# Optimization experiments

Measured on AMD Instinct MI355X. Metric: run time of the kernel, lower is better.

Reference implementation:

```python
import jax, jax.numpy as jnp
from jax import lax
import numpy as np

B, S, V, E, H, K = 128, 512, 32000, 128, 128, 32  # H = hidden_dim//2 per direction
START, END = 30, 31


def _lstm_dir(x, h0, c0, W_ih, W_hh, b):
    # x: [S, B, E]; PyTorch gate order: i, f, g, o
    def step(carry, xt):
        h, c = carry
        gates = xt @ W_ih.T + h @ W_hh.T + b  # [B, 4H]
        i, f, g, o = jnp.split(gates, 4, axis=1)
        c = jax.nn.sigmoid(f) * c + jax.nn.sigmoid(i) * jnp.tanh(g)
        h = jax.nn.sigmoid(o) * jnp.tanh(c)
        return (h, c), h
    _, hs = lax.scan(step, (h0, c0), x)
    return hs  # [S, B, H]


def _get_features(sentence, embed_table, W_ih_f, W_hh_f, b_ih_f, b_hh_f,
                  W_ih_b, W_hh_b, b_ih_b, b_hh_b, W_out, b_out, h0, c0):
    emb = embed_table[sentence]            # [B, S, E]
    x = emb.transpose(1, 0, 2)             # [S, B, E]
    hf = _lstm_dir(x, h0[0], c0[0], W_ih_f, W_hh_f, b_ih_f + b_hh_f)
    hb = _lstm_dir(x[::-1], h0[1], c0[1], W_ih_b, W_hh_b, b_ih_b + b_hh_b)[::-1]
    out = jnp.concatenate([hf, hb], axis=-1).transpose(1, 0, 2)  # [B, S, 2H]
    return out @ W_out.T + b_out           # [B, S, K]


def _numerator(feats, tags, transitions):
    b = tags.shape[0]
    start = jnp.full((b, 1), START, dtype=tags.dtype)
    ext = jnp.concatenate([start, tags], axis=1)  # [B, S+1]
    trans = transitions[ext[:, :-1], ext[:, 1:]].sum(axis=1)
    emit = jnp.take_along_axis(feats, tags[:, :, None], axis=2)[..., 0].sum(axis=1)
    return trans + emit + transitions[tags[:, -1], END]


def _denominator(feats, transitions):
    b, _, k = feats.shape
    init = jnp.full((b, k), -10000.0, feats.dtype).at[:, START].set(0.0)
    def step(alpha, feat):
        # alpha[b, prev]; transitions[next, prev] (as in the torch code)
        new = jax.nn.logsumexp(alpha[:, None, :] + transitions[None, :, :], axis=2) + feat
        return new, None
    alpha, _ = lax.scan(step, init, feats.transpose(1, 0, 2))
    return jax.nn.logsumexp(alpha + transitions[:, END][None, :], axis=1)


def setup_inputs():
    key = jax.random.key(0)
    ks = jax.random.split(key, 16)
    n = lambda k, shape, s=0.1: jax.random.normal(k, shape, jnp.float32) * s
    sentence = jax.random.randint(ks[0], (B, S), 0, V)
    tags = jax.random.randint(ks[1], (B, S), 0, START)
    transitions = n(ks[13], (K, K), 0.1)
    transitions = transitions.at[:, START].set(-10000.0).at[END, :].set(-10000.0)
    return dict(
        sentence=sentence, tags=tags,
        embed_table=n(ks[2], (V, E), 1.0),
        W_ih_f=n(ks[3], (4 * H, E)), W_hh_f=n(ks[4], (4 * H, H)),
        b_ih_f=n(ks[5], (4 * H,)), b_hh_f=n(ks[6], (4 * H,)),
        W_ih_b=n(ks[7], (4 * H, E)), W_hh_b=n(ks[8], (4 * H, H)),
        b_ih_b=n(ks[9], (4 * H,)), b_hh_b=n(ks[10], (4 * H,)),
        W_out=n(ks[11], (K, 2 * H)), b_out=n(ks[12], (K,)),
        transitions=transitions,
        h0=n(ks[14], (2, B, H)), c0=n(ks[15], (2, B, H)),
    )


def reference(sentence, tags, embed_table, W_ih_f, W_hh_f, b_ih_f, b_hh_f,
              W_ih_b, W_hh_b, b_ih_b, b_hh_b, W_out, b_out, transitions, h0, c0):
    feats = _get_features(sentence, embed_table, W_ih_f, W_hh_f, b_ih_f, b_hh_f,
                          W_ih_b, W_hh_b, b_ih_b, b_hh_b, W_out, b_out, h0, c0)
    num = _numerator(feats, tags, transitions)
    den = _denominator(feats, transitions)
    return jnp.mean(num - den)
```

## Files before the change

kernel.cpp:

```cpp
#include <hip/hip_runtime.h>

typedef unsigned int uint;
typedef __fp16 half2_t __attribute__((ext_vector_type(2)));
typedef __fp16 half8_t __attribute__((ext_vector_type(8)));
typedef float floatx4 __attribute__((ext_vector_type(4)));

#define SEQ 512
#define BATCH 128
#define HID 128
#define NTAG 32
#define START_TAG 30
#define END_TAG 31

__device__ __forceinline__ float fdot2(uint a, uint b, float c) {
  return __builtin_amdgcn_fdot2(__builtin_bit_cast(half2_t, a),
                                __builtin_bit_cast(half2_t, b), c, false);
}
__device__ __forceinline__ uint packh2(float a, float b) {
  half2_t h = __builtin_amdgcn_cvt_pkrtz(a, b);
  return __builtin_bit_cast(uint, h);
}
__device__ __forceinline__ float frcp(float x) { return __builtin_amdgcn_rcpf(x); }
__device__ __forceinline__ float fsig(float x) { return frcp(1.f + __expf(-x)); }
__device__ __forceinline__ float ftanh(float x) { return 1.f - 2.f * frcp(1.f + __expf(2.f * x)); }
__device__ __forceinline__ float fexp2(float x) { return __builtin_amdgcn_exp2f(x); }
__device__ __forceinline__ float flog2(float x) { return __builtin_amdgcn_logf(x); }

__global__ __launch_bounds__(256) void prep_kernel(
    const float* __restrict__ Wihf, const float* __restrict__ Whhf,
    const float* __restrict__ bihf, const float* __restrict__ bhhf,
    const float* __restrict__ Wihb, const float* __restrict__ Whhb,
    const float* __restrict__ bihb, const float* __restrict__ bhhb,
    const float* __restrict__ Wout,
    uint* __restrict__ wihI, uint* __restrict__ whh,
    uint* __restrict__ woutp, float* __restrict__ biasI)
{
  int idx = blockIdx.x * 256 + threadIdx.x;
  if (idx < 65536) {
    int d = idx >> 15, rem = idx & 32767;
    int n = rem >> 6, dw = rem & 63;
    int m = n >> 2, q = n & 3;
    int g = q * 128 + m;
    const float* W = d ? Wihb : Wihf;
    wihI[idx] = packh2(W[g * 128 + 2 * dw], W[g * 128 + 2 * dw + 1]);
  }
  int i2 = idx - 65536;
  if (i2 >= 0 && i2 < 65536) {
    int d = i2 >> 15, rem = i2 & 32767;
    int g = rem >> 6, dw = rem & 63;
    const float* W = d ? Whhb : Whhf;
    whh[i2] = packh2(W[g * 128 + 2 * dw], W[g * 128 + 2 * dw + 1]);
  }
  int i3 = idx - 131072;
  if (i3 >= 0 && i3 < 4096) {
    int k = i3 >> 7, dw = i3 & 127;
    float a, b2;
    if (dw < 64) { a = Wout[k * 256 + 2 * dw]; b2 = Wout[k * 256 + 2 * dw + 1]; }
    else { int j = dw - 64; a = Wout[k * 256 + 128 + 2 * j]; b2 = Wout[k * 256 + 128 + 2 * j + 1]; }
    woutp[i3] = packh2(a, b2);
  }
  int i4 = idx - 135168;
  if (i4 >= 0 && i4 < 1024) {
    int d = i4 >> 9, n = i4 & 511;
    int g = (n & 3) * 128 + (n >> 2);
    biasI[i4] = d ? (bihb[g] + bhhb[g]) : (bihf[g] + bhhf[g]);
  }
}

__global__ __launch_bounds__(256, 2) void gemmx_kernel(
    const int* __restrict__ sentence, const float* __restrict__ embed,
    const uint* __restrict__ wihI, const float* __restrict__ biasI,
    uint* __restrict__ gatex, int chunk)
{
  int blk = blockIdx.x;
  int tl = blk & 127, nb = (blk >> 7) & 3, d = blk >> 9;
  int t = chunk * 128 + tl;
  int s = d ? (511 - t) : t;
  __shared__ int tok[128];
  int tid = threadIdx.x;
  if (tid < 128) tok[tid] = sentence[tid * SEQ + s];
  __syncthreads();

  int w = tid >> 6, lane = tid & 63;
  int q = lane >> 4, r = lane & 15;
  int wr = w >> 1, wc = w & 1;
  int r0 = wr * 64;
  int c0 = nb * 128 + wc * 64;

  floatx4 acc[4][4];
#pragma unroll
  for (int i = 0; i < 4; ++i)
#pragma unroll
    for (int j = 0; j < 4; ++j) acc[i][j] = (floatx4){0.f, 0.f, 0.f, 0.f};

  const float4* aptr[4];
#pragma unroll
  for (int i = 0; i < 4; ++i)
    aptr[i] = (const float4*)(embed + (size_t)tok[r0 + i * 16 + r] * HID) + q * 2;
  const uint4* bptr[4];
#pragma unroll
  for (int j = 0; j < 4; ++j)
    bptr[j] = (const uint4*)(wihI + ((size_t)d * 512 + c0 + j * 16 + r) * 64) + q;

#pragma unroll
  for (int kc = 0; kc < 4; ++kc) {
    half8_t af[4], bf[4];
#pragma unroll
    for (int i = 0; i < 4; ++i) {
      float4 x0 = aptr[i][kc * 8];
      float4 x1 = aptr[i][kc * 8 + 1];
      uint4 u;
      u.x = packh2(x0.x, x0.y); u.y = packh2(x0.z, x0.w);
      u.z = packh2(x1.x, x1.y); u.w = packh2(x1.z, x1.w);
      af[i] = __builtin_bit_cast(half8_t, u);
    }
#pragma unroll
    for (int j = 0; j < 4; ++j)
      bf[j] = __builtin_bit_cast(half8_t, bptr[j][kc * 4]);
#pragma unroll
    for (int i = 0; i < 4; ++i)
#pragma unroll
      for (int j = 0; j < 4; ++j)
        acc[i][j] = __builtin_amdgcn_mfma_f32_16x16x32_f16(af[i], bf[j], acc[i][j], 0, 0, 0);
  }

  __fp16* gat = ((__fp16*)gatex) + (size_t)d * 16384 * 512;
#pragma unroll
  for (int j = 0; j < 4; ++j) {
    int n = c0 + j * 16 + r;
    float bb = biasI[d * 512 + n];
#pragma unroll
    for (int i = 0; i < 4; ++i) {
      int rb = r0 + i * 16 + q * 4;
#pragma unroll
      for (int reg = 0; reg < 4; ++reg) {
        float v = acc[i][j][reg] + bb;
        gat[((size_t)(tl * 128 + rb + reg)) * 512 + n] = (__fp16)v;
      }
    }
  }
}

__global__ __launch_bounds__(256, 1) void lstm_kernel(
    const uint* __restrict__ gatex, const uint* __restrict__ whh,
    const float* __restrict__ h0, const float* __restrict__ c0,
    float* __restrict__ statec, uint* __restrict__ hh, int chunk)
{
  const int wg = blockIdx.x;
  const int d = wg >> 7, b = wg & 127;
  const int tid = threadIdx.x;
  const int w = tid >> 6, lane = tid & 63;
  const int hp = lane >> 5, r = lane & 31;
  const int m = w * 32 + r;

  __shared__ __align__(16) __fp16 hist[128][128];
  __shared__ uint occupancy_pad[16384];
  if (chunk == -12345) occupancy_pad[tid] = (uint)tid;

  const uint4* wh4 = (const uint4*)(whh + (size_t)d * 512 * 64);
  uint4 wreg[4][8];
#pragma unroll
  for (int q = 0; q < 4; ++q) {
    const uint4* row = wh4 + (q * 128 + m) * 16 + hp * 8;
#pragma unroll
    for (int i = 0; i < 8; ++i) wreg[q][i] = row[i];
  }

  float c = (chunk == 0) ? c0[(size_t)(d * 128 + b) * 128 + m]
                         : statec[(size_t)(d * 128 + b) * 128 + m];

  if (tid < 64) {
    uint* h127 = (uint*)&hist[127][0];
    if (chunk == 0) {
      float2 hv = ((const float2*)(h0 + (size_t)(d * 128 + b) * 128))[tid];
      h127[tid] = packh2(hv.x, hv.y);
    } else {
      int sprev = d ? (511 - (chunk * 128 - 1)) : (chunk * 128 - 1);
      h127[tid] = hh[((size_t)(d * 512 + sprev) * 128 + b) * 64 + tid];
    }
  }
  const uint* gx0 = gatex + (size_t)d * 4194304 + (size_t)b * 256 + 2 * m;
  uint2 gx = *(const uint2*)(gx0);
  __syncthreads();

  for (int tl = 0; tl < 128; ++tl) {
    uint2 gxn = gx;
    if (tl < 127) gxn = *(const uint2*)(gx0 + (size_t)(tl + 1) * 32768);

    float a0 = 0.f, a1 = 0.f, a2 = 0.f, a3 = 0.f;
    const uint4* z4 = (const uint4*)(&hist[(tl + 127) & 127][hp * 64]);
#pragma unroll
    for (int i = 0; i < 8; ++i) {
      uint4 z = z4[i];
      a0 = fdot2(z.x, wreg[0][i].x, a0);
      a0 = fdot2(z.y, wreg[0][i].y, a0);
      a0 = fdot2(z.z, wreg[0][i].z, a0);
      a0 = fdot2(z.w, wreg[0][i].w, a0);
      a1 = fdot2(z.x, wreg[1][i].x, a1);
      a1 = fdot2(z.y, wreg[1][i].y, a1);
      a1 = fdot2(z.z, wreg[1][i].z, a1);
      a1 = fdot2(z.w, wreg[1][i].w, a1);
      a2 = fdot2(z.x, wreg[2][i].x, a2);
      a2 = fdot2(z.y, wreg[2][i].y, a2);
      a2 = fdot2(z.z, wreg[2][i].z, a2);
      a2 = fdot2(z.w, wreg[2][i].w, a2);
      a3 = fdot2(z.x, wreg[3][i].x, a3);
      a3 = fdot2(z.y, wreg[3][i].y, a3);
      a3 = fdot2(z.z, wreg[3][i].z, a3);
      a3 = fdot2(z.w, wreg[3][i].w, a3);
    }
    a0 += __shfl_xor(a0, 32);
    a1 += __shfl_xor(a1, 32);
    a2 += __shfl_xor(a2, 32);
    a3 += __shfl_xor(a3, 32);

    half2_t g01 = __builtin_bit_cast(half2_t, gx.x);
    half2_t g23 = __builtin_bit_cast(half2_t, gx.y);
    a0 += (float)g01[0];
    a1 += (float)g01[1];
    a2 += (float)g23[0];
    a3 += (float)g23[1];

    float ig = fsig(a0);
    float fg = fsig(a1);
    float gg = ftanh(a2);
    float og = fsig(a3);
    c = fg * c + ig * gg;
    float hv = og * ftanh(c);

    if (hp == 0) hist[tl][m] = (__fp16)hv;
    gx = gxn;
    __syncthreads();
  }

  statec[(size_t)(d * 128 + b) * 128 + m] = c;

  int base = chunk * 128;
  for (int i = tid; i < 2048; i += 256) {
    int sl = i >> 4, q4 = i & 15;
    int s = d ? (511 - (base + sl)) : (base + sl);
    *(uint4*)(&hh[((size_t)(d * 512 + s) * 128 + b) * 64 + q4 * 4]) =
        *(const uint4*)((const uint*)&hist[sl][0] + q4 * 4);
  }
}

__global__ __launch_bounds__(256) void outproj_kernel(
    const uint* __restrict__ hh, const uint* __restrict__ woutp,
    const float* __restrict__ bout, float* __restrict__ feats)
{
  __shared__ __align__(16) uint4 zrow[8][32];
  __shared__ __align__(16) uint4 wlds[32][32];
  int tid = threadIdx.x;
  for (int j = tid; j < 1024; j += 256) {
    int k = j >> 5, i = j & 31;
    wlds[i][k] = ((const uint4*)woutp)[j];
  }
  int rl = tid >> 5, q = tid & 31;
  int row = blockIdx.x * 8 + rl;
  int b = row >> 9, s = row & 511;
  const uint4* hf4 = (const uint4*)(hh + ((size_t)s * BATCH + b) * 64);
  const uint4* hb4 = (const uint4*)(hh + ((size_t)(SEQ + s) * BATCH + b) * 64);
  zrow[rl][q] = (q < 16) ? hf4[q] : hb4[q - 16];
  __syncthreads();
  int k = q;
  float acc = bout[k];
#pragma unroll
  for (int i = 0; i < 32; ++i) {
    uint4 z = zrow[rl][i];
    uint4 wv = wlds[i][k];
    acc = fdot2(z.x, wv.x, acc);
    acc = fdot2(z.y, wv.y, acc);
    acc = fdot2(z.z, wv.z, acc);
    acc = fdot2(z.w, wv.w, acc);
  }
  feats[(size_t)row * 32 + k] = acc;
}

__global__ __launch_bounds__(64) void crf_num_kernel(
    const int* __restrict__ tags, const float* __restrict__ feats,
    const float* __restrict__ trans, float* __restrict__ num)
{
  int b = blockIdx.x, l = threadIdx.x;
  const int* tb = tags + b * SEQ;
  float acc = 0.f;
  for (int s = l; s < SEQ; s += 64) {
    int tg = tb[s];
    int pv = (s == 0) ? START_TAG : tb[s - 1];
    acc += trans[pv * NTAG + tg] + feats[((size_t)b * SEQ + s) * NTAG + tg];
  }
#pragma unroll
  for (int msk = 1; msk < 64; msk <<= 1) acc += __shfl_xor(acc, msk);
  if (l == 0) num[b] = acc + trans[tb[SEQ - 1] * NTAG + END_TAG];
}

__global__ __launch_bounds__(64) void crf_seg_kernel(
    const float* __restrict__ feats, const float* __restrict__ trans,
    uint* __restrict__ segP, float* __restrict__ segL)
{
  const float L2E = 1.4426950408889634f;
  int blk = blockIdx.x;
  int b = blk >> 5, j = blk & 31;
  int tstart = 1 + 16 * j;
  int nsteps = (j == 31) ? 15 : 16;
  int lane = threadIdx.x;
  int c = lane & 15, q = lane >> 4;

  half8_t afr[2];
#pragma unroll
  for (int rt = 0; rt < 2; ++rt) {
    const float* trow = trans + (rt * 16 + c) * 32 + q * 8;
    float e[8];
#pragma unroll
    for (int i = 0; i < 8; ++i) e[i] = fexp2(trow[i] * L2E);
    uint4 u;
    u.x = packh2(e[0], e[1]); u.y = packh2(e[2], e[3]);
    u.z = packh2(e[4], e[5]); u.w = packh2(e[6], e[7]);
    afr[rt] = __builtin_bit_cast(half8_t, u);
  }
  half8_t bfr[2];
#pragma unroll
  for (int ct = 0; ct < 2; ++ct) {
    uint4 u;
    uint vals[8];
#pragma unroll
    for (int i = 0; i < 8; ++i)
      vals[i] = ((q * 8 + i) == (ct * 16 + c)) ? 0x3C00u : 0u;
    u.x = vals[0] | (vals[1] << 16);
    u.y = vals[2] | (vals[3] << 16);
    u.z = vals[4] | (vals[5] << 16);
    u.w = vals[6] | (vals[7] << 16);
    bfr[ct] = __builtin_bit_cast(half8_t, u);
  }

  __shared__ __fp16 P16[32 * 36];

  const float* fb = feats + ((size_t)b * SEQ + tstart) * NTAG;
  float Lacc = 0.f;
  float4 pre0 = *(const float4*)(fb + q * 4);
  float4 pre1 = *(const float4*)(fb + 16 + q * 4);

  for (int s = 0; s < nsteps; ++s) {
    float4 f0 = pre0, f1 = pre1;
    if (s + 1 < nsteps) {
      pre0 = *(const float4*)(fb + (s + 1) * 32 + q * 4);
      pre1 = *(const float4*)(fb + (s + 1) * 32 + 16 + q * 4);
    }
    floatx4 z4 = (floatx4){0.f, 0.f, 0.f, 0.f};
    floatx4 c00 = __builtin_amdgcn_mfma_f32_16x16x32_f16(afr[0], bfr[0], z4, 0, 0, 0);
    floatx4 c01 = __builtin_amdgcn_mfma_f32_16x16x32_f16(afr[0], bfr[1], z4, 0, 0, 0);
    floatx4 c10 = __builtin_amdgcn_mfma_f32_16x16x32_f16(afr[1], bfr[0], z4, 0, 0, 0);
    floatx4 c11 = __builtin_amdgcn_mfma_f32_16x16x32_f16(afr[1], bfr[1], z4, 0, 0, 0);
    float pf0[4], pf1[4];
    pf0[0] = fexp2(f0.x * L2E); pf0[1] = fexp2(f0.y * L2E);
    pf0[2] = fexp2(f0.z * L2E); pf0[3] = fexp2(f0.w * L2E);
    pf1[0] = fexp2(f1.x * L2E); pf1[1] = fexp2(f1.y * L2E);
    pf1[2] = fexp2(f1.z * L2E); pf1[3] = fexp2(f1.w * L2E);
    float v00[4], v01[4], v10[4], v11[4];
#pragma unroll
    for (int rg = 0; rg < 4; ++rg) {
      v00[rg] = c00[rg] * pf0[rg];
      v01[rg] = c01[rg] * pf0[rg];
      v10[rg] = c10[rg] * pf1[rg];
      v11[rg] = c11[rg] * pf1[rg];
    }
    float mx = 0.f;
#pragma unroll
    for (int rg = 0; rg < 4; ++rg)
      mx = fmaxf(mx, fmaxf(fmaxf(v00[rg], v01[rg]), fmaxf(v10[rg], v11[rg])));
    uint ub = (uint)__builtin_amdgcn_readfirstlane((int)__builtin_bit_cast(uint, mx));
    int e = (int)((ub >> 23) & 255u);
    Lacc += (float)(e - 127);
    float sc = __builtin_bit_cast(float, (uint)((254 - e) << 23));

    __syncthreads();
    {
      uint2 wv2;
      wv2.x = packh2(v00[0] * sc, v00[1] * sc);
      wv2.y = packh2(v00[2] * sc, v00[3] * sc);
      *(uint2*)(&P16[c * 36 + q * 4]) = wv2;
      wv2.x = packh2(v10[0] * sc, v10[1] * sc);
      wv2.y = packh2(v10[2] * sc, v10[3] * sc);
      *(uint2*)(&P16[c * 36 + 16 + q * 4]) = wv2;
      wv2.x = packh2(v01[0] * sc, v01[1] * sc);
      wv2.y = packh2(v01[2] * sc, v01[3] * sc);
      *(uint2*)(&P16[(16 + c) * 36 + q * 4]) = wv2;
      wv2.x = packh2(v11[0] * sc, v11[1] * sc);
      wv2.y = packh2(v11[2] * sc, v11[3] * sc);
      *(uint2*)(&P16[(16 + c) * 36 + 16 + q * 4]) = wv2;
    }
    __syncthreads();
    {
      uint2 lo0 = *(const uint2*)(&P16[c * 36 + q * 8]);
      uint2 hi0 = *(const uint2*)(&P16[c * 36 + q * 8 + 4]);
      uint4 u0; u0.x = lo0.x; u0.y = lo0.y; u0.z = hi0.x; u0.w = hi0.y;
      bfr[0] = __builtin_bit_cast(half8_t, u0);
      uint2 lo1 = *(const uint2*)(&P16[(16 + c) * 36 + q * 8]);
      uint2 hi1 = *(const uint2*)(&P16[(16 + c) * 36 + q * 8 + 4]);
      uint4 u1; u1.x = lo1.x; u1.y = lo1.y; u1.z = hi1.x; u1.w = hi1.y;
      bfr[1] = __builtin_bit_cast(half8_t, u1);
    }
  }
  __syncthreads();
  uint* gp = segP + (size_t)blk * 512;
  if (lane < 32) {
    int i = lane;
#pragma unroll
    for (int tp = 0; tp < 16; ++tp) {
      uint lo = (uint)__builtin_bit_cast(unsigned short, P16[(2 * tp) * 36 + i]);
      uint hi = (uint)__builtin_bit_cast(unsigned short, P16[(2 * tp + 1) * 36 + i]);
      gp[i * 16 + tp] = lo | (hi << 16);
    }
  }
  if (lane == 0) segL[blk] = Lacc;
}

__global__ __launch_bounds__(64) void crf_comb_kernel(
    const float* __restrict__ feats, const float* __restrict__ trans,
    const uint* __restrict__ segP, const float* __restrict__ segL,
    float* __restrict__ den)
{
  const float L2E = 1.4426950408889634f, LN2 = 0.6931471805599453f;
  int b = blockIdx.x, l = threadIdx.x;
  int i = l & 31, hp = l >> 5;
  const float* fb = feats + (size_t)b * SEQ * NTAG;

  float sT = 0.f;
  for (int p = 0; p < 32; ++p) sT += fexp2(trans[i * 32 + p] * L2E);
  float v = (1.f + sT) * fexp2(fb[i] * L2E);
  float L = -10000.f * L2E;

  float vo = __shfl_xor(v, 1);
  uint pv = (i & 1) ? packh2(vo, v) : packh2(v, vo);

  const uint* gp0 = segP + (size_t)b * 32 * 512 + i * 16 + hp * 8;
  uint4 ra = *(const uint4*)(gp0);
  uint4 rb = *(const uint4*)(gp0 + 4);

  for (int seg = 0; seg < 32; ++seg) {
    uint4 ca = ra, cb = rb;
    if (seg + 1 < 32) {
      ra = *(const uint4*)(gp0 + (seg + 1) * 512);
      rb = *(const uint4*)(gp0 + (seg + 1) * 512 + 4);
    }
    float g0 = __shfl(__builtin_bit_cast(float, pv), hp * 16 + 0);
    float g1 = __shfl(__builtin_bit_cast(float, pv), hp * 16 + 2);
    float g2 = __shfl(__builtin_bit_cast(float, pv), hp * 16 + 4);
    float g3 = __shfl(__builtin_bit_cast(float, pv), hp * 16 + 6);
    float g4 = __shfl(__builtin_bit_cast(float, pv), hp * 16 + 8);
    float g5 = __shfl(__builtin_bit_cast(float, pv), hp * 16 + 10);
    float g6 = __shfl(__builtin_bit_cast(float, pv), hp * 16 + 12);
    float g7 = __shfl(__builtin_bit_cast(float, pv), hp * 16 + 14);
    float acc = 0.f;
    acc = fdot2(__builtin_bit_cast(uint, g0), ca.x, acc);
    acc = fdot2(__builtin_bit_cast(uint, g1), ca.y, acc);
    acc = fdot2(__builtin_bit_cast(uint, g2), ca.z, acc);
    acc = fdot2(__builtin_bit_cast(uint, g3), ca.w, acc);
    acc = fdot2(__builtin_bit_cast(uint, g4), cb.x, acc);
    acc = fdot2(__builtin_bit_cast(uint, g5), cb.y, acc);
    acc = fdot2(__builtin_bit_cast(uint, g6), cb.z, acc);
    acc = fdot2(__builtin_bit_cast(uint, g7), cb.w, acc);
    float sm = acc + __shfl_xor(acc, 32);
    uint ub = (uint)__builtin_amdgcn_readfirstlane((int)__builtin_bit_cast(uint, sm));
    int e = (int)((ub >> 23) & 255u);
    L += (float)(e - 127) + segL[b * 32 + seg];
    float sc = __builtin_bit_cast(float, (uint)((254 - e) << 23));
    v = sm * sc;
    float vo2 = __shfl_xor(v, 1);
    pv = (i & 1) ? packh2(vo2, v) : packh2(v, vo2);
  }
  float wv = v * fexp2(trans[i * 32 + END_TAG] * L2E);
#pragma unroll
  for (int msk = 1; msk <= 16; msk <<= 1) wv += __shfl_xor(wv, msk);
  if (l == 0) den[b] = (L + flog2(wv)) * LN2;
}

__global__ __launch_bounds__(128) void final_kernel(
    const float* __restrict__ num, const float* __restrict__ den,
    float* __restrict__ out)
{
  int tid = threadIdx.x;
  float v = num[tid] - den[tid];
#pragma unroll
  for (int msk = 1; msk < 64; msk <<= 1) v += __shfl_xor(v, msk);
  __shared__ float tmp[2];
  if ((tid & 63) == 0) tmp[tid >> 6] = v;
  __syncthreads();
  if (tid == 0) out[0] = (tmp[0] + tmp[1]) * (1.f / 128.f);
}

extern "C" void kernel_launch(void* const* d_in, const int* in_sizes, int n_in,
                              void* d_out, int out_size, void* d_ws, size_t ws_size,
                              hipStream_t stream)
{
  const int* sentence = (const int*)d_in[0];
  const int* tags = (const int*)d_in[1];
  const float* embed = (const float*)d_in[2];
  const float* Wihf = (const float*)d_in[3];
  const float* Whhf = (const float*)d_in[4];
  const float* bihf = (const float*)d_in[5];
  const float* bhhf = (const float*)d_in[6];
  const float* Wihb = (const float*)d_in[7];
  const float* Whhb = (const float*)d_in[8];
  const float* bihb = (const float*)d_in[9];
  const float* bhhb = (const float*)d_in[10];
  const float* Wout = (const float*)d_in[11];
  const float* bout = (const float*)d_in[12];
  const float* trans = (const float*)d_in[13];
  const float* h0 = (const float*)d_in[14];
  const float* c0 = (const float*)d_in[15];
  float* out = (float*)d_out;

  char* ws = (char*)d_ws;
  uint* wihI = (uint*)(ws + 0);
  uint* whh = (uint*)(ws + 262144);
  uint* woutp = (uint*)(ws + 524288);
  float* biasI = (float*)(ws + 540672);
  float* numb = (float*)(ws + 544768);
  float* denb = (float*)(ws + 545280);
  float* statec = (float*)(ws + 545792);
  uint* hh = (uint*)(ws + 1048576);
  uint* gatex = (uint*)(ws + 34603008);
  float* feats = (float*)(ws + 34603008);
  uint* segP = (uint*)(ws + 42991616);
  float* segL = (float*)(ws + 51380224);

  hipLaunchKernelGGL(prep_kernel, dim3(532), dim3(256), 0, stream,
                     Wihf, Whhf, bihf, bhhf, Wihb, Whhb, bihb, bhhb, Wout,
                     wihI, whh, woutp, biasI);
  for (int c = 0; c < 4; ++c) {
    hipLaunchKernelGGL(gemmx_kernel, dim3(1024), dim3(256), 0, stream,
                       sentence, embed, wihI, biasI, gatex, c);
    hipLaunchKernelGGL(lstm_kernel, dim3(256), dim3(256), 0, stream,
                       gatex, whh, h0, c0, statec, hh, c);
  }
  hipLaunchKernelGGL(outproj_kernel, dim3(8192), dim3(256), 0, stream,
                     hh, woutp, bout, feats);
  hipLaunchKernelGGL(crf_num_kernel, dim3(128), dim3(64), 0, stream,
                     tags, feats, trans, numb);
  hipLaunchKernelGGL(crf_seg_kernel, dim3(4096), dim3(64), 0, stream,
                     feats, trans, segP, segL);
  hipLaunchKernelGGL(crf_comb_kernel, dim3(128), dim3(64), 0, stream,
                     feats, trans, segP, segL, denb);
  hipLaunchKernelGGL(final_kernel, dim3(1), dim3(128), 0, stream,
                     numb, denb, out);
}
```

Before: 579.3 us.

## Split LSTM recurrent dot product four ways across 512 threads per block

The LSTM recurrence kernel now uses 512 threads per block instead of 256. Each hidden unit's 128-long recurrent dot product is split across four lanes rather than two, and the partial sums are combined with two xor shuffles. This halves the per-thread weight registers and the serial fdot2 chain on each time step's critical path. The LDS padding array that forced one block per CU is replaced by a waves-per-EU attribute. The cost is more waves taking part in every per-step barrier and extra shuffle latency.

```diff
diff --git a/kernel.cpp b/kernel.cpp
--- a/kernel.cpp
+++ b/kernel.cpp
@@ -141,7 +141,8 @@
   }
 }
 
-__global__ __launch_bounds__(256, 1) void lstm_kernel(
+__global__ __attribute__((amdgpu_waves_per_eu(2, 2))) __launch_bounds__(512)
+void lstm_kernel(
     const uint* __restrict__ gatex, const uint* __restrict__ whh,
     const float* __restrict__ h0, const float* __restrict__ c0,
     float* __restrict__ statec, uint* __restrict__ hh, int chunk)
@@ -149,21 +150,17 @@
   const int wg = blockIdx.x;
   const int d = wg >> 7, b = wg & 127;
   const int tid = threadIdx.x;
-  const int w = tid >> 6, lane = tid & 63;
-  const int hp = lane >> 5, r = lane & 31;
-  const int m = w * 32 + r;
+  const int kq = tid & 3, m = tid >> 2;
 
   __shared__ __align__(16) __fp16 hist[128][128];
-  __shared__ uint occupancy_pad[16384];
-  if (chunk == -12345) occupancy_pad[tid] = (uint)tid;
-
-  const uint4* wh4 = (const uint4*)(whh + (size_t)d * 512 * 64);
-  uint4 wreg[4][8];
-#pragma unroll
-  for (int q = 0; q < 4; ++q) {
-    const uint4* row = wh4 + (q * 128 + m) * 16 + hp * 8;
-#pragma unroll
-    for (int i = 0; i < 8; ++i) wreg[q][i] = row[i];
+
+  const uint4* wh4 = (const uint4*)whh + (size_t)d * 8192;
+  uint4 wreg[4][4];
+#pragma unroll
+  for (int g = 0; g < 4; ++g) {
+    const uint4* row = wh4 + ((size_t)(g * 128 + m)) * 16 + kq * 4;
+#pragma unroll
+    for (int i = 0; i < 4; ++i) wreg[g][i] = row[i];
   }
 
   float c = (chunk == 0) ? c0[(size_t)(d * 128 + b) * 128 + m]
@@ -188,9 +185,9 @@
     if (tl < 127) gxn = *(const uint2*)(gx0 + (size_t)(tl + 1) * 32768);
 
     float a0 = 0.f, a1 = 0.f, a2 = 0.f, a3 = 0.f;
-    const uint4* z4 = (const uint4*)(&hist[(tl + 127) & 127][hp * 64]);
-#pragma unroll
-    for (int i = 0; i < 8; ++i) {
+    const uint4* z4 = (const uint4*)(&hist[(tl + 127) & 127][kq * 32]);
+#pragma unroll
+    for (int i = 0; i < 4; ++i) {
       uint4 z = z4[i];
       a0 = fdot2(z.x, wreg[0][i].x, a0);
       a0 = fdot2(z.y, wreg[0][i].y, a0);
@@ -209,10 +206,10 @@
       a3 = fdot2(z.z, wreg[3][i].z, a3);
       a3 = fdot2(z.w, wreg[3][i].w, a3);
     }
-    a0 += __shfl_xor(a0, 32);
-    a1 += __shfl_xor(a1, 32);
-    a2 += __shfl_xor(a2, 32);
-    a3 += __shfl_xor(a3, 32);
+    a0 += __shfl_xor(a0, 1); a0 += __shfl_xor(a0, 2);
+    a1 += __shfl_xor(a1, 1); a1 += __shfl_xor(a1, 2);
+    a2 += __shfl_xor(a2, 1); a2 += __shfl_xor(a2, 2);
+    a3 += __shfl_xor(a3, 1); a3 += __shfl_xor(a3, 2);
 
     half2_t g01 = __builtin_bit_cast(half2_t, gx.x);
     half2_t g23 = __builtin_bit_cast(half2_t, gx.y);
@@ -228,15 +225,15 @@
     c = fg * c + ig * gg;
     float hv = og * ftanh(c);
 
-    if (hp == 0) hist[tl][m] = (__fp16)hv;
+    if (kq == 0) hist[tl][m] = (__fp16)hv;
     gx = gxn;
     __syncthreads();
   }
 
-  statec[(size_t)(d * 128 + b) * 128 + m] = c;
+  if (kq == 0) statec[(size_t)(d * 128 + b) * 128 + m] = c;
 
   int base = chunk * 128;
-  for (int i = tid; i < 2048; i += 256) {
+  for (int i = tid; i < 2048; i += 512) {
     int sl = i >> 4, q4 = i & 15;
     int s = d ? (511 - (base + sl)) : (base + sl);
     *(uint4*)(&hh[((size_t)(d * 512 + s) * 128 + b) * 64 + q4 * 4]) =
@@ -530,7 +527,7 @@
   for (int c = 0; c < 4; ++c) {
     hipLaunchKernelGGL(gemmx_kernel, dim3(1024), dim3(256), 0, stream,
                        sentence, embed, wihI, biasI, gatex, c);
-    hipLaunchKernelGGL(lstm_kernel, dim3(256), dim3(256), 0, stream,
+    hipLaunchKernelGGL(lstm_kernel, dim3(256), dim3(512), 0, stream,
                        gatex, whh, h0, c0, statec, hh, c);
   }
   hipLaunchKernelGGL(outproj_kernel, dim3(8192), dim3(256), 0, stream,
```

After: 627.2 us. 1.08x slower.
